# Kernel optimization log

Measured on AMD Instinct MI355X. Metric: run time of the kernel, lower is better.

## Reference

```python
import jax, jax.numpy as jnp
import numpy as np

N_HEAD = 16
HEAD_SIZE = 64
N_EMBD = 1024
B, T = 4, 2048
THETA = 10000.0


def _rope_cos_sin(t_len, dim):
    # freqs: (dim//2,), angles: (T, dim//2)
    inv = 1.0 / (THETA ** (jnp.arange(0, dim, 2, dtype=jnp.float32) / dim))
    ang = jnp.arange(t_len, dtype=jnp.float32)[:, None] * inv[None, :]
    return jnp.cos(ang), jnp.sin(ang)


def _apply_rope(x, cos, sin):
    # x: (B, H, T, hs) -> complex-pair rotation over last dim
    xr = x.reshape(*x.shape[:-1], -1, 2)
    x0, x1 = xr[..., 0], xr[..., 1]
    c = cos[None, None, :, :]
    s = sin[None, None, :, :]
    o0 = x0 * c - x1 * s
    o1 = x0 * s + x1 * c
    return jnp.stack([o0, o1], axis=-1).reshape(x.shape)


def setup_inputs() -> dict:
    key = jax.random.key(0)
    ks = jax.random.split(key, 5)
    scale = 1.0 / np.sqrt(N_EMBD)
    return {
        "x": jax.random.normal(ks[0], (B, T, N_EMBD), dtype=jnp.float32),
        "Wq": jax.random.normal(ks[1], (N_EMBD, N_HEAD * HEAD_SIZE), dtype=jnp.float32) * scale,
        "Wk": jax.random.normal(ks[2], (N_EMBD, N_HEAD * HEAD_SIZE), dtype=jnp.float32) * scale,
        "Wv": jax.random.normal(ks[3], (N_EMBD, N_HEAD * HEAD_SIZE), dtype=jnp.float32) * scale,
        "Wp": jax.random.normal(ks[4], (N_HEAD * HEAD_SIZE, N_EMBD), dtype=jnp.float32) * scale,
        "bp": jnp.zeros((N_EMBD,), dtype=jnp.float32),
    }


def reference(x, Wq, Wk, Wv, Wp, bp):
    Bx, Tx, C = x.shape
    q = (x @ Wq).reshape(Bx, Tx, N_HEAD, HEAD_SIZE).transpose(0, 2, 1, 3)
    k = (x @ Wk).reshape(Bx, Tx, N_HEAD, HEAD_SIZE).transpose(0, 2, 1, 3)
    v = (x @ Wv).reshape(Bx, Tx, N_HEAD, HEAD_SIZE).transpose(0, 2, 1, 3)
    cos, sin = _rope_cos_sin(Tx, HEAD_SIZE)
    q = _apply_rope(q, cos, sin)
    k = _apply_rope(k, cos, sin)
    wei = jnp.einsum('bhqd,bhkd->bhqk', q, k) * (HEAD_SIZE ** -0.5)
    causal = jnp.tril(jnp.ones((Tx, Tx), dtype=bool))
    wei = jnp.where(causal[None, None, :, :], wei, -jnp.inf)
    wei = jax.nn.softmax(wei, axis=-1)
    out = jnp.einsum('bhqk,bhkd->bhqd', wei, v)
    out = out.transpose(0, 2, 1, 3).reshape(Bx, Tx, N_HEAD * HEAD_SIZE)
    return out @ Wp + bp
```

## Files before the change

### kernel.cpp

```cpp
#include <hip/hip_runtime.h>
#include <hip/hip_bf16.h>

#define NH 16
#define HS 64
#define CE 1024
#define BB 4
#define TT 2048

typedef __bf16 bf16;
typedef __bf16 v8bf __attribute__((ext_vector_type(8)));
typedef __bf16 v4bf __attribute__((ext_vector_type(4)));
typedef __bf16 v2bf __attribute__((ext_vector_type(2)));
typedef float v4f __attribute__((ext_vector_type(4)));
typedef float v16f __attribute__((ext_vector_type(16)));

#define GLD16(gp, lp)                                                              \
    __builtin_amdgcn_global_load_lds((const __attribute__((address_space(1))) void*)(gp), \
                                     (__attribute__((address_space(3))) void*)(lp), 16, 0, 0)

__global__ __launch_bounds__(256) void cast_x_kernel(const float* __restrict__ x,
                                                     bf16* __restrict__ xb) {
    int idx = (blockIdx.x * 256 + threadIdx.x) * 8;
    const float4* xp = (const float4*)(x + idx);
    float4 a = xp[0], b = xp[1];
    v8bf o;
    o[0] = (bf16)a.x; o[1] = (bf16)a.y; o[2] = (bf16)a.z; o[3] = (bf16)a.w;
    o[4] = (bf16)b.x; o[5] = (bf16)b.y; o[6] = (bf16)b.z; o[7] = (bf16)b.w;
    *(v8bf*)(xb + idx) = o;
}

__global__ __launch_bounds__(256) void transpose_w_kernel(const float* __restrict__ W0,
                                                          const float* __restrict__ W1,
                                                          const float* __restrict__ W2,
                                                          const float* __restrict__ W3,
                                                          bf16* __restrict__ dqkv,
                                                          bf16* __restrict__ dp) {
    __shared__ bf16 tile[64][66];
    int z = blockIdx.z;
    const float* W = (z == 0) ? W0 : (z == 1) ? W1 : (z == 2) ? W2 : W3;
    bf16* Wt = (z < 3) ? (dqkv + (size_t)z * 1024 * CE) : dp;
    int k0 = blockIdx.x * 64;
    int n0 = blockIdx.y * 64;
    int tx = threadIdx.x & 63;
    int ty = threadIdx.x >> 6;
    for (int s = 0; s < 16; s++) {
        int r = s * 4 + ty;
        tile[r][tx] = (bf16)W[(size_t)(k0 + r) * CE + n0 + tx];
    }
    __syncthreads();
    for (int s = 0; s < 16; s++) {
        int r = s * 4 + ty;
        Wt[(size_t)(n0 + r) * CE + k0 + tx] = tile[tx][r];
    }
}

template <int MODE>
__global__ __launch_bounds__(256) void gemm_bt(const bf16* __restrict__ A,
                                               const bf16* __restrict__ Bt,
                                               bf16* __restrict__ Qb_, bf16* __restrict__ Kb_,
                                               bf16* __restrict__ Vt_,
                                               float* __restrict__ Pout,
                                               const float* __restrict__ bias) {
    __shared__ __align__(16) bf16 As[128 * 64];
    __shared__ __align__(16) bf16 Bs[128 * 64];
    const int tid = threadIdx.x;
    const int lane = tid & 63, wave = tid >> 6;
    const int lane15 = lane & 15, quad = lane >> 4;
    const int wr = wave >> 1, wc = wave & 1;
    const int m0 = blockIdx.y * 128;
    const int n0 = blockIdx.x * 128;

    v4f acc[4][4] = {};

    const int cm = tid >> 3;
    const int ck = (tid & 7) * 8;
    const bf16* Ag = A + (size_t)(m0 + cm) * CE + ck;
    const bf16* Bg = Bt + (size_t)(n0 + cm) * CE + ck;
    bf16* aD = &As[wave * 512];
    bf16* bD = &Bs[wave * 512];

    for (int k0 = 0; k0 < CE; k0 += 64) {
        __syncthreads();
#pragma unroll
        for (int p = 0; p < 4; p++) GLD16(Ag + k0 + (size_t)(p * 32) * CE, aD + p * 2048);
#pragma unroll
        for (int p = 0; p < 4; p++) GLD16(Bg + k0 + (size_t)(p * 32) * CE, bD + p * 2048);
        __syncthreads();
#pragma unroll
        for (int kh = 0; kh < 2; kh++) {
            v8bf af[4], bfr[4];
            for (int i = 0; i < 4; i++)
                af[i] = *(const v8bf*)(&As[(wr * 64 + i * 16 + lane15) * 64 + kh * 32 + quad * 8]);
            for (int j = 0; j < 4; j++)
                bfr[j] = *(const v8bf*)(&Bs[(wc * 64 + j * 16 + lane15) * 64 + kh * 32 + quad * 8]);
            for (int i = 0; i < 4; i++)
                for (int j = 0; j < 4; j++)
                    acc[i][j] = __builtin_amdgcn_mfma_f32_16x16x32_bf16(af[i], bfr[j], acc[i][j], 0, 0, 0);
        }
    }

    for (int i = 0; i < 4; i++) {
        for (int j = 0; j < 4; j++) {
            int gmb = m0 + wr * 64 + i * 16 + quad * 4;
            int gn = n0 + wc * 64 + j * 16 + lane15;
            if (MODE == 1) {
                float bb = bias[gn];
                for (int r = 0; r < 4; r++)
                    Pout[(size_t)(gmb + r) * CE + gn] = acc[i][j][r] + bb;
            } else {
                int w = gn >> 10;
                int n = gn & 1023;
                int h = n >> 6, d = n & 63;
                if (w < 2) {
                    bf16* out = w ? Kb_ : Qb_;
                    for (int r = 0; r < 4; r++) {
                        int gm = gmb + r;
                        int b = gm >> 11, t = gm & 2047;
                        out[(((size_t)(b * NH + h)) * TT + t) * HS + d] = (bf16)acc[i][j][r];
                    }
                } else {
                    int b = gmb >> 11, t = gmb & 2047;
                    v4bf pack;
                    for (int r = 0; r < 4; r++) pack[r] = (bf16)acc[i][j][r];
                    *(v4bf*)(&Vt_[(((size_t)(b * NH + h)) * HS + d) * TT + t]) = pack;
                }
            }
        }
    }
}

__global__ __launch_bounds__(256) void rope_kernel(bf16* __restrict__ Qb, bf16* __restrict__ Kb) {
    unsigned idx = blockIdx.x * 256 + threadIdx.x;
    bool isK = blockIdx.y != 0;
    bf16* buf = isK ? Kb : Qb;
    int i = idx & 31;
    int t = (idx >> 5) & 2047;
    float inv = exp2f(-0.41524101186092034f * (float)i);
    float ang = (float)t * inv;
    float s, c;
    sincosf(ang, &s, &c);
    if (!isK) { s *= 0.125f; c *= 0.125f; }
    bf16* p = buf + (size_t)idx * 2;
    v2bf v = *(v2bf*)p;
    float x0 = (float)v[0], x1 = (float)v[1];
    v2bf o;
    o[0] = (bf16)(x0 * c - x1 * s);
    o[1] = (bf16)(x0 * s + x1 * c);
    *(v2bf*)p = o;
}

__global__ __launch_bounds__(256, 2) void attn_kernel(const bf16* __restrict__ Qb,
                                                      const bf16* __restrict__ Kb,
                                                      const bf16* __restrict__ Vt,
                                                      bf16* __restrict__ Ob) {
    __shared__ __align__(16) bf16 Ks[32 * 64];
    __shared__ __align__(16) bf16 Vs[64 * 32];
    const int tid = threadIdx.x, lane = tid & 63, wave = tid >> 6;
    const int lane31 = lane & 31, h = lane >> 5;
    const int pair = blockIdx.x >> 6;
    const int bh = blockIdx.x & 63;
    const int q0A = pair * 128 + wave * 32;
    const int q0B = (15 - pair) * 128 + wave * 32;
    const bf16* Qp = Qb + (size_t)bh * TT * HS;
    const bf16* Kp = Kb + (size_t)bh * TT * HS;
    const bf16* Vp = Vt + (size_t)bh * HS * TT;

    v8bf qfA[4], qfB[4];
    for (int m = 0; m < 4; m++) {
        qfA[m] = *(const v8bf*)(Qp + (q0A + lane31) * HS + m * 16 + h * 8);
        qfB[m] = *(const v8bf*)(Qp + (q0B + lane31) * HS + m * 16 + h * 8);
    }

    v16f oA0 = {}, oA1 = {}, oB0 = {}, oB1 = {};
    float mA = -3.0e38f, lA = 0.f, mB = -3.0e38f, lB = 0.f;

    const int kr = tid >> 3, kc = tid & 7;
    const bf16* kg = Kp + kr * HS + ((kc ^ (kr & 7)) * 8);
    const int vd = tid >> 2, vc = tid & 3;
    const bf16* vg = Vp + (size_t)vd * TT + ((vc ^ (vd & 3)) * 8);
    bf16* ksDst = &Ks[wave * 512];
    bf16* vsDst = &Vs[wave * 512];

    v8bf kf[4], vf[2][2];

    auto step = [&](const v8bf* qf, v16f& o0, v16f& o1, float& m_i, float& l_i, bool diag) {
        v16f s = {};
        for (int m = 0; m < 4; m++)
            s = __builtin_amdgcn_mfma_f32_32x32x16_bf16(kf[m], qf[m], s, 0, 0, 0);
        float p[16];
        for (int r = 0; r < 16; r++) {
            float v = s[r];
            if (diag) {
                int kvr = (r & 3) + 8 * (r >> 2) + 4 * h;
                v = (kvr <= lane31) ? v : -3.0e38f;
            }
            p[r] = v;
        }
        float t8[8];
        for (int r = 0; r < 8; r++) t8[r] = fmaxf(p[r], p[r + 8]);
        float mx = fmaxf(fmaxf(fmaxf(t8[0], t8[1]), fmaxf(t8[2], t8[3])),
                         fmaxf(fmaxf(t8[4], t8[5]), fmaxf(t8[6], t8[7])));
        mx = fmaxf(mx, __shfl_xor(mx, 32));
        bool anyUpd = __ballot(mx > m_i) != 0ull;
        float mn = fmaxf(m_i, mx);
        for (int r = 0; r < 16; r++) p[r] = __expf(p[r] - mn);
        float a8[8];
        for (int r = 0; r < 8; r++) a8[r] = p[r] + p[r + 8];
        float rs = ((a8[0] + a8[1]) + (a8[2] + a8[3])) + ((a8[4] + a8[5]) + (a8[6] + a8[7]));
        rs += __shfl_xor(rs, 32);
        if (anyUpd) {
            float alpha = __expf(m_i - mn);
            m_i = mn;
            l_i = l_i * alpha + rs;
            for (int r = 0; r < 16; r++) { o0[r] *= alpha; o1[r] *= alpha; }
        } else {
            l_i += rs;
        }
        union { v4bf v; unsigned long long u; } ch[4];
        for (int g = 0; g < 4; g++)
            for (int rr = 0; rr < 4; rr++)
                ch[g].v[rr] = (bf16)p[g * 4 + rr];
        for (int t = 0; t < 2; t++) {
            unsigned long long mine0 = ch[2 * t].u, mine1 = ch[2 * t + 1].u;
            unsigned long long send = h ? mine0 : mine1;
            unsigned long long recv = __shfl_xor(send, 32);
            union { v8bf v; unsigned long long u[2]; } bfr;
            bfr.u[0] = h ? recv : mine0;
            bfr.u[1] = h ? mine1 : recv;
            o0 = __builtin_amdgcn_mfma_f32_32x32x16_bf16(vf[t][0], bfr.v, o0, 0, 0, 0);
            o1 = __builtin_amdgcn_mfma_f32_32x32x16_bf16(vf[t][1], bfr.v, o1, 0, 0, 0);
        }
    };

    const int kv_end = (15 - pair) * 128 + 96;
    for (int kv0 = 0; kv0 <= kv_end; kv0 += 32) {
        __syncthreads();
        GLD16(kg + kv0 * HS, ksDst);
        GLD16(vg + kv0, vsDst);
        __syncthreads();
        for (int m = 0; m < 4; m++)
            kf[m] = *(const v8bf*)(&Ks[lane31 * 64 + (((m << 1) | h) ^ (lane31 & 7)) * 8]);
        for (int t = 0; t < 2; t++)
            for (int dh = 0; dh < 2; dh++)
                vf[t][dh] = *(const v8bf*)(&Vs[(dh * 32 + lane31) * 32 + ((((t << 1) | h) ^ (lane31 & 3)) * 8)]);
        if (kv0 <= q0B) step(qfB, oB0, oB1, mB, lB, kv0 == q0B);
        if (kv0 <= q0A) step(qfA, oA0, oA1, mA, lA, kv0 == q0A);
    }

    const int b = bh >> 4, hh = bh & 15;
    auto writeO = [&](int q0, v16f& o0, v16f& o1, float l_i) {
        int q = q0 + lane31;
        float invl = 1.f / l_i;
        bf16* outRow = Ob + ((size_t)(b * TT + q)) * CE + hh * HS;
        for (int g = 0; g < 4; g++) {
            v4bf w0, w1;
            for (int rr = 0; rr < 4; rr++) {
                w0[rr] = (bf16)(o0[g * 4 + rr] * invl);
                w1[rr] = (bf16)(o1[g * 4 + rr] * invl);
            }
            *(v4bf*)(outRow + g * 8 + h * 4) = w0;
            *(v4bf*)(outRow + 32 + g * 8 + h * 4) = w1;
        }
    };
    writeO(q0A, oA0, oA1, lA);
    writeO(q0B, oB0, oB1, lB);
}

extern "C" void kernel_launch(void* const* d_in, const int* in_sizes, int n_in,
                              void* d_out, int out_size, void* d_ws, size_t ws_size,
                              hipStream_t stream) {
    const float* x  = (const float*)d_in[0];
    const float* Wq = (const float*)d_in[1];
    const float* Wk = (const float*)d_in[2];
    const float* Wv = (const float*)d_in[3];
    const float* Wp = (const float*)d_in[4];
    const float* bp = (const float*)d_in[5];
    char* ws = (char*)d_ws;
    const size_t MB = 1024 * 1024;
    bf16* Xb    = (bf16*)(ws);
    bf16* WqkvT = (bf16*)(ws + 16 * MB);
    bf16* WpT   = (bf16*)(ws + 22 * MB);
    bf16* Qb    = (bf16*)(ws + 24 * MB);
    bf16* Kb    = (bf16*)(ws + 40 * MB);
    bf16* Vt    = (bf16*)(ws + 56 * MB);
    bf16* Ob    = (bf16*)(ws + 72 * MB);

    cast_x_kernel<<<dim3(4096), dim3(256), 0, stream>>>(x, Xb);
    transpose_w_kernel<<<dim3(16, 16, 4), dim3(256), 0, stream>>>(Wq, Wk, Wv, Wp, WqkvT, WpT);

    gemm_bt<0><<<dim3(24, 64), dim3(256), 0, stream>>>(Xb, WqkvT, Qb, Kb, Vt, nullptr, nullptr);

    rope_kernel<<<dim3(16384, 2), dim3(256), 0, stream>>>(Qb, Kb);

    attn_kernel<<<dim3(512), dim3(256), 0, stream>>>(Qb, Kb, Vt, Ob);

    gemm_bt<1><<<dim3(8, 64), dim3(256), 0, stream>>>(Ob, WpT, nullptr, nullptr, nullptr,
                                                      (float*)d_out, bp);
}
```

Measured before the change: 302.4 us.

## Split attention to one q-block per workgroup, swizzle GEMM LDS, use exp2

The attention kernel now gives each workgroup a single 128-row query block instead of a paired front/back block, doubling the grid to 1024 workgroups and raising the launch-bounds occupancy hint to 4. K and V fragments are read from LDS right where they are used, which cuts register pressure. The query scale now folds in log2(e) so softmax can use the hardware exp2. The GEMM LDS tiles get an XOR swizzle to avoid bank conflicts. Risks: the block mapping is less balanced than the pairing, and blocks with shorter causal ranges may finish at uneven times.

```diff
diff --git a/kernel.cpp b/kernel.cpp
--- a/kernel.cpp
+++ b/kernel.cpp
@@ -17,6 +17,12 @@
 #define GLD16(gp, lp)                                                              \
     __builtin_amdgcn_global_load_lds((const __attribute__((address_space(1))) void*)(gp), \
                                      (__attribute__((address_space(3))) void*)(lp), 16, 0, 0)
+
+#if __has_builtin(__builtin_amdgcn_exp2f)
+#define EXP2(x) __builtin_amdgcn_exp2f(x)
+#else
+#define EXP2(x) exp2f(x)
+#endif
 
 __global__ __launch_bounds__(256) void cast_x_kernel(const float* __restrict__ x,
                                                      bf16* __restrict__ xb) {
@@ -73,7 +79,7 @@
     v4f acc[4][4] = {};
 
     const int cm = tid >> 3;
-    const int ck = (tid & 7) * 8;
+    const int ck = ((tid & 7) ^ (cm & 7)) * 8;
     const bf16* Ag = A + (size_t)(m0 + cm) * CE + ck;
     const bf16* Bg = Bt + (size_t)(n0 + cm) * CE + ck;
     bf16* aD = &As[wave * 512];
@@ -89,10 +95,14 @@
 #pragma unroll
         for (int kh = 0; kh < 2; kh++) {
             v8bf af[4], bfr[4];
-            for (int i = 0; i < 4; i++)
-                af[i] = *(const v8bf*)(&As[(wr * 64 + i * 16 + lane15) * 64 + kh * 32 + quad * 8]);
-            for (int j = 0; j < 4; j++)
-                bfr[j] = *(const v8bf*)(&Bs[(wc * 64 + j * 16 + lane15) * 64 + kh * 32 + quad * 8]);
+            for (int i = 0; i < 4; i++) {
+                int row = wr * 64 + i * 16 + lane15;
+                af[i] = *(const v8bf*)(&As[row * 64 + (((kh * 4 + quad) ^ (lane15 & 7)) * 8)]);
+            }
+            for (int j = 0; j < 4; j++) {
+                int row = wc * 64 + j * 16 + lane15;
+                bfr[j] = *(const v8bf*)(&Bs[row * 64 + (((kh * 4 + quad) ^ (lane15 & 7)) * 8)]);
+            }
             for (int i = 0; i < 4; i++)
                 for (int j = 0; j < 4; j++)
                     acc[i][j] = __builtin_amdgcn_mfma_f32_16x16x32_bf16(af[i], bfr[j], acc[i][j], 0, 0, 0);
@@ -139,7 +149,10 @@
     float ang = (float)t * inv;
     float s, c;
     sincosf(ang, &s, &c);
-    if (!isK) { s *= 0.125f; c *= 0.125f; }
+    if (!isK) {
+        const float QS = 0.18033688011112042f;
+        s *= QS; c *= QS;
+    }
     bf16* p = buf + (size_t)idx * 2;
     v2bf v = *(v2bf*)p;
     float x0 = (float)v[0], x1 = (float)v[1];
@@ -149,7 +162,7 @@
     *(v2bf*)p = o;
 }
 
-__global__ __launch_bounds__(256, 2) void attn_kernel(const bf16* __restrict__ Qb,
+__global__ __launch_bounds__(256, 4) void attn_kernel(const bf16* __restrict__ Qb,
                                                       const bf16* __restrict__ Kb,
                                                       const bf16* __restrict__ Vt,
                                                       bf16* __restrict__ Ob) {
@@ -157,22 +170,21 @@
     __shared__ __align__(16) bf16 Vs[64 * 32];
     const int tid = threadIdx.x, lane = tid & 63, wave = tid >> 6;
     const int lane31 = lane & 31, h = lane >> 5;
-    const int pair = blockIdx.x >> 6;
     const int bh = blockIdx.x & 63;
-    const int q0A = pair * 128 + wave * 32;
-    const int q0B = (15 - pair) * 128 + wave * 32;
+    const int base = (blockIdx.x >> 6) & 3;
+    const int g = blockIdx.x >> 8;
+    const int qb = (g == 0) ? base : (g == 1) ? 7 - base : (g == 2) ? 8 + base : 15 - base;
+    const int q0 = qb * 128 + wave * 32;
     const bf16* Qp = Qb + (size_t)bh * TT * HS;
     const bf16* Kp = Kb + (size_t)bh * TT * HS;
     const bf16* Vp = Vt + (size_t)bh * HS * TT;
 
-    v8bf qfA[4], qfB[4];
-    for (int m = 0; m < 4; m++) {
-        qfA[m] = *(const v8bf*)(Qp + (q0A + lane31) * HS + m * 16 + h * 8);
-        qfB[m] = *(const v8bf*)(Qp + (q0B + lane31) * HS + m * 16 + h * 8);
-    }
-
-    v16f oA0 = {}, oA1 = {}, oB0 = {}, oB1 = {};
-    float mA = -3.0e38f, lA = 0.f, mB = -3.0e38f, lB = 0.f;
+    v8bf qf[4];
+    for (int m = 0; m < 4; m++)
+        qf[m] = *(const v8bf*)(Qp + (q0 + lane31) * HS + m * 16 + h * 8);
+
+    v16f o0 = {}, o1 = {};
+    float m_i = -3.0e38f, l_i = 0.f;
 
     const int kr = tid >> 3, kc = tid & 7;
     const bf16* kg = Kp + kr * HS + ((kc ^ (kr & 7)) * 8);
@@ -181,12 +193,21 @@
     bf16* ksDst = &Ks[wave * 512];
     bf16* vsDst = &Vs[wave * 512];
 
-    v8bf kf[4], vf[2][2];
-
-    auto step = [&](const v8bf* qf, v16f& o0, v16f& o1, float& m_i, float& l_i, bool diag) {
+    const int kv_max = qb * 128 + 96;
+    for (int kv0 = 0; kv0 <= kv_max; kv0 += 32) {
+        __syncthreads();
+        GLD16(kg + kv0 * HS, ksDst);
+        GLD16(vg + kv0, vsDst);
+        __syncthreads();
+        if (kv0 > q0) continue;
+        const bool diag = (kv0 == q0);
+
         v16f s = {};
-        for (int m = 0; m < 4; m++)
-            s = __builtin_amdgcn_mfma_f32_32x32x16_bf16(kf[m], qf[m], s, 0, 0, 0);
+        for (int m = 0; m < 4; m++) {
+            v8bf af = *(const v8bf*)(&Ks[lane31 * 64 + (((m << 1) | h) ^ (lane31 & 7)) * 8]);
+            s = __builtin_amdgcn_mfma_f32_32x32x16_bf16(af, qf[m], s, 0, 0, 0);
+        }
+
         float p[16];
         for (int r = 0; r < 16; r++) {
             float v = s[r];
@@ -203,23 +224,25 @@
         mx = fmaxf(mx, __shfl_xor(mx, 32));
         bool anyUpd = __ballot(mx > m_i) != 0ull;
         float mn = fmaxf(m_i, mx);
-        for (int r = 0; r < 16; r++) p[r] = __expf(p[r] - mn);
+        for (int r = 0; r < 16; r++) p[r] = EXP2(p[r] - mn);
         float a8[8];
         for (int r = 0; r < 8; r++) a8[r] = p[r] + p[r + 8];
         float rs = ((a8[0] + a8[1]) + (a8[2] + a8[3])) + ((a8[4] + a8[5]) + (a8[6] + a8[7]));
         rs += __shfl_xor(rs, 32);
         if (anyUpd) {
-            float alpha = __expf(m_i - mn);
+            float alpha = EXP2(m_i - mn);
             m_i = mn;
             l_i = l_i * alpha + rs;
             for (int r = 0; r < 16; r++) { o0[r] *= alpha; o1[r] *= alpha; }
         } else {
             l_i += rs;
         }
+
         union { v4bf v; unsigned long long u; } ch[4];
-        for (int g = 0; g < 4; g++)
+        for (int gg = 0; gg < 4; gg++)
             for (int rr = 0; rr < 4; rr++)
-                ch[g].v[rr] = (bf16)p[g * 4 + rr];
+                ch[gg].v[rr] = (bf16)p[gg * 4 + rr];
+
         for (int t = 0; t < 2; t++) {
             unsigned long long mine0 = ch[2 * t].u, mine1 = ch[2 * t + 1].u;
             unsigned long long send = h ? mine0 : mine1;
@@ -227,43 +250,27 @@
             union { v8bf v; unsigned long long u[2]; } bfr;
             bfr.u[0] = h ? recv : mine0;
             bfr.u[1] = h ? mine1 : recv;
-            o0 = __builtin_amdgcn_mfma_f32_32x32x16_bf16(vf[t][0], bfr.v, o0, 0, 0, 0);
-            o1 = __builtin_amdgcn_mfma_f32_32x32x16_bf16(vf[t][1], bfr.v, o1, 0, 0, 0);
-        }
-    };
-
-    const int kv_end = (15 - pair) * 128 + 96;
-    for (int kv0 = 0; kv0 <= kv_end; kv0 += 32) {
-        __syncthreads();
-        GLD16(kg + kv0 * HS, ksDst);
-        GLD16(vg + kv0, vsDst);
-        __syncthreads();
-        for (int m = 0; m < 4; m++)
-            kf[m] = *(const v8bf*)(&Ks[lane31 * 64 + (((m << 1) | h) ^ (lane31 & 7)) * 8]);
-        for (int t = 0; t < 2; t++)
-            for (int dh = 0; dh < 2; dh++)
-                vf[t][dh] = *(const v8bf*)(&Vs[(dh * 32 + lane31) * 32 + ((((t << 1) | h) ^ (lane31 & 3)) * 8)]);
-        if (kv0 <= q0B) step(qfB, oB0, oB1, mB, lB, kv0 == q0B);
-        if (kv0 <= q0A) step(qfA, oA0, oA1, mA, lA, kv0 == q0A);
+            int cidx = (((t << 1) | h) ^ (lane31 & 3)) * 8;
+            v8bf va0 = *(const v8bf*)(&Vs[lane31 * 32 + cidx]);
+            o0 = __builtin_amdgcn_mfma_f32_32x32x16_bf16(va0, bfr.v, o0, 0, 0, 0);
+            v8bf va1 = *(const v8bf*)(&Vs[(32 + lane31) * 32 + cidx]);
+            o1 = __builtin_amdgcn_mfma_f32_32x32x16_bf16(va1, bfr.v, o1, 0, 0, 0);
+        }
     }
 
     const int b = bh >> 4, hh = bh & 15;
-    auto writeO = [&](int q0, v16f& o0, v16f& o1, float l_i) {
-        int q = q0 + lane31;
-        float invl = 1.f / l_i;
-        bf16* outRow = Ob + ((size_t)(b * TT + q)) * CE + hh * HS;
-        for (int g = 0; g < 4; g++) {
-            v4bf w0, w1;
-            for (int rr = 0; rr < 4; rr++) {
-                w0[rr] = (bf16)(o0[g * 4 + rr] * invl);
-                w1[rr] = (bf16)(o1[g * 4 + rr] * invl);
-            }
-            *(v4bf*)(outRow + g * 8 + h * 4) = w0;
-            *(v4bf*)(outRow + 32 + g * 8 + h * 4) = w1;
-        }
-    };
-    writeO(q0A, oA0, oA1, lA);
-    writeO(q0B, oB0, oB1, lB);
+    const int q = q0 + lane31;
+    float invl = 1.f / l_i;
+    bf16* outRow = Ob + ((size_t)(b * TT + q)) * CE + hh * HS;
+    for (int gg = 0; gg < 4; gg++) {
+        v4bf w0, w1;
+        for (int rr = 0; rr < 4; rr++) {
+            w0[rr] = (bf16)(o0[gg * 4 + rr] * invl);
+            w1[rr] = (bf16)(o1[gg * 4 + rr] * invl);
+        }
+        *(v4bf*)(outRow + gg * 8 + h * 4) = w0;
+        *(v4bf*)(outRow + 32 + gg * 8 + h * 4) = w1;
+    }
 }
 
 extern "C" void kernel_launch(void* const* d_in, const int* in_sizes, int n_in,
@@ -292,7 +299,7 @@
 
     rope_kernel<<<dim3(16384, 2), dim3(256), 0, stream>>>(Qb, Kb);
 
-    attn_kernel<<<dim3(512), dim3(256), 0, stream>>>(Qb, Kb, Vt, Ob);
+    attn_kernel<<<dim3(1024), dim3(256), 0, stream>>>(Qb, Kb, Vt, Ob);
 
     gemm_bt<1><<<dim3(8, 64), dim3(256), 0, stream>>>(Ob, WpT, nullptr, nullptr, nullptr,
                                                       (float*)d_out, bp);
```

Result: faster. 276.9 us (-8.4%).
